# Performance work log

Hardware: AMD Instinct MI355X
Metric: run time of the kernel (lower is better)

## Reference

```python
import jax, jax.numpy as jnp
import numpy as np

HEADS = 8


def setup_inputs() -> dict:
    key = jax.random.key(0)
    ks = jax.random.split(key, 6)
    B, N, D = 4, 2048, 512
    return {
        "x": jax.random.normal(ks[0], (B, N, D), dtype=jnp.float32),
        "pos": jax.random.uniform(ks[1], (B, N, 3), dtype=jnp.float32),
        "qkv_w": jax.random.normal(ks[2], (3 * D, D), dtype=jnp.float32) * 0.02,
        "qkv_b": jax.random.normal(ks[3], (3 * D,), dtype=jnp.float32) * 0.02,
        "out_w": jax.random.normal(ks[4], (D, D), dtype=jnp.float32) * 0.02,
        "out_b": jax.random.normal(ks[5], (D,), dtype=jnp.float32) * 0.02,
    }


def reference(x, pos, qkv_w, qkv_b, out_w, out_b):
    B, N, D = x.shape
    H = HEADS
    Dh = D // H
    scale = D ** (-0.5)  # NOTE: original uses full dim, not head dim

    # QKV projection -> [3, B, H, N, Dh]
    qkv = (x @ qkv_w.T + qkv_b).reshape(B, N, 3, H, Dh).transpose(2, 0, 3, 1, 4)
    q, k, v = qkv[0], qkv[1], qkv[2]

    # partial 3D RoPE on first 6 head dims (3 axis pairs)
    theta = pos * jnp.pi                    # [B, N, 3]
    sin = jnp.sin(theta)[:, None]           # [B, 1, N, 3] broadcasts over heads
    cos = jnp.cos(theta)[:, None]

    def rotate(t):
        x_rot = t[..., :6]
        x1 = x_rot[..., 0::2]               # [B, H, N, 3]
        x2 = x_rot[..., 1::2]
        return jnp.concatenate(
            [x1 * cos - x2 * sin, x1 * sin + x2 * cos, t[..., 6:]], axis=-1
        )

    q = rotate(q)
    k = rotate(k)

    attn = jax.nn.softmax(jnp.einsum("bhqd,bhkd->bhqk", q, k) * scale, axis=-1)
    out = jnp.einsum("bhqk,bhkd->bhqd", attn, v)          # [B, H, N, Dh]
    out = out.transpose(0, 2, 1, 3).reshape(B, N, D)
    return out @ out_w.T + out_b
```

## Files before the change

### kernel.cpp

```cpp
#include <hip/hip_runtime.h>
#include <stdint.h>

typedef __attribute__((ext_vector_type(4))) float f32x4;
typedef __attribute__((ext_vector_type(16))) float f32x16;
typedef __attribute__((ext_vector_type(8))) short bf16x8;
typedef __attribute__((ext_vector_type(4))) unsigned short u16x4;

__device__ __forceinline__ unsigned short f2bf(float f) {
    unsigned int u = __builtin_bit_cast(unsigned int, f);
    u += 0x7fffu + ((u >> 16) & 1u);
    return (unsigned short)(u >> 16);
}
__device__ __forceinline__ float bf2f(unsigned short s) {
    unsigned int u = ((unsigned int)s) << 16;
    return __builtin_bit_cast(float, u);
}
__device__ __forceinline__ float fexp2(float x) {
#if __has_builtin(__builtin_amdgcn_exp2f)
    return __builtin_amdgcn_exp2f(x);
#else
    return exp2f(x);
#endif
}
__device__ __forceinline__ unsigned int cvt_pk_bf16(float lo, float hi) {
    unsigned int r;
    asm("v_cvt_pk_bf16_f32 %0, %1, %2" : "=v"(r) : "v"(lo), "v"(hi));
    return r;
}

__global__ void k_cvt3(const float* __restrict__ x,
                       const float* __restrict__ w1,
                       const float* __restrict__ w2,
                       unsigned short* __restrict__ out) {
    const int C1 = 1048576;
    const int C2 = 196608;
    int i = blockIdx.x * blockDim.x + threadIdx.x;
    f32x4 v;
    if (i < C1)            v = ((const f32x4*)x)[i];
    else if (i < C1 + C2)  v = ((const f32x4*)w1)[i - C1];
    else                   v = ((const f32x4*)w2)[i - C1 - C2];
    u16x4 o;
    o.x = f2bf(v.x); o.y = f2bf(v.y); o.z = f2bf(v.z); o.w = f2bf(v.w);
    ((u16x4*)out)[i] = o;
}

template<int OUT_BF16>
__global__ __launch_bounds__(256, 2)
void k_gemm_nt(const unsigned short* __restrict__ A,
               const unsigned short* __restrict__ Bm,
               const float* __restrict__ bias,
               void* __restrict__ Cout, int M, int N, int K) {
    __shared__ unsigned short As[128 * 64];
    __shared__ unsigned short Bs[128 * 64];
    const int tid = threadIdx.x;
    const int lane = tid & 63;
    const int w = tid >> 6;
    const int wr = (w >> 1) * 64, wc = (w & 1) * 64;
    const int g = lane >> 4, fr = lane & 15;

    f32x4 acc[4][4];
#pragma unroll
    for (int i = 0; i < 4; ++i)
#pragma unroll
        for (int j = 0; j < 4; ++j) acc[i][j] = f32x4{0.f, 0.f, 0.f, 0.f};

    const int srow8 = lane >> 3;
    const int swc = ((lane & 7) ^ srow8) * 8;
    const unsigned short* Abase = A + (size_t)(blockIdx.x * 128 + w * 8 + srow8) * K + swc;
    const unsigned short* Bbase = Bm + (size_t)(blockIdx.y * 128 + w * 8 + srow8) * K + swc;
    char* ldsA = (char*)As + w * 1024;
    char* ldsB = (char*)Bs + w * 1024;

    for (int k0 = 0; k0 < K; k0 += 64) {
        __syncthreads();
#pragma unroll
        for (int i = 0; i < 4; ++i) {
            __builtin_amdgcn_global_load_lds(
                (const __attribute__((address_space(1))) void*)(Abase + (size_t)i * 32 * K + k0),
                (__attribute__((address_space(3))) void*)(ldsA + i * 4096), 16, 0, 0);
            __builtin_amdgcn_global_load_lds(
                (const __attribute__((address_space(1))) void*)(Bbase + (size_t)i * 32 * K + k0),
                (__attribute__((address_space(3))) void*)(ldsB + i * 4096), 16, 0, 0);
        }
        __syncthreads();
        bf16x8 af[2][4], bfv[2][4];
#pragma unroll
        for (int kk = 0; kk < 2; ++kk) {
#pragma unroll
            for (int mi = 0; mi < 4; ++mi)
                af[kk][mi] = *(const bf16x8*)&As[(wr + mi * 16 + fr) * 64 + (((kk * 4 + g) ^ (fr & 7)) * 8)];
#pragma unroll
            for (int ni = 0; ni < 4; ++ni)
                bfv[kk][ni] = *(const bf16x8*)&Bs[(wc + ni * 16 + fr) * 64 + (((kk * 4 + g) ^ (fr & 7)) * 8)];
        }
#pragma unroll
        for (int kk = 0; kk < 2; ++kk)
#pragma unroll
            for (int mi = 0; mi < 4; ++mi)
#pragma unroll
                for (int ni = 0; ni < 4; ++ni)
                    acc[mi][ni] = __builtin_amdgcn_mfma_f32_16x16x32_bf16(af[kk][mi], bfv[kk][ni], acc[mi][ni], 0, 0, 0);
    }

#pragma unroll
    for (int mi = 0; mi < 4; ++mi) {
#pragma unroll
        for (int ni = 0; ni < 4; ++ni) {
            int row = blockIdx.x * 128 + wr + mi * 16 + g * 4;
            int col = blockIdx.y * 128 + wc + ni * 16 + fr;
            float bz = bias[col];
#pragma unroll
            for (int r = 0; r < 4; ++r) {
                float v = acc[mi][ni][r] + bz;
                if (OUT_BF16) ((unsigned short*)Cout)[(size_t)(row + r) * N + col] = f2bf(v);
                else          ((float*)Cout)[(size_t)(row + r) * N + col] = v;
            }
        }
    }
}

__global__ void k_rotary(const unsigned short* __restrict__ qkv,
                         const float* __restrict__ pos,
                         unsigned short* __restrict__ Qb,
                         unsigned short* __restrict__ Kb,
                         unsigned short* __restrict__ VT) {
    const float PI = 3.14159265358979323846f;
    const float QS = 0.04419417382415922f * 1.44269504088896341f;
    int cid = blockIdx.x * 256 + threadIdx.x;
    int s = cid >> 19;
    int r = cid & 524287;
    if (s < 2) {
        int m = r >> 6, c = r & 63;
        int h = c >> 3, dc = c & 7;
        int b = m >> 11, n = m & 2047;
        bf16x8 v = *(const bf16x8*)&qkv[m * 1536 + s * 512 + c * 8];
        float f[8];
#pragma unroll
        for (int i = 0; i < 8; ++i) f[i] = bf2f((unsigned short)v[i]);
        if (dc == 0) {
            float nf[6];
#pragma unroll
            for (int j = 0; j < 3; ++j) {
                float th = pos[m * 3 + j] * PI;
                float sn = __sinf(th), cs = __cosf(th);
                float x1 = f[2 * j], x2 = f[2 * j + 1];
                nf[j] = x1 * cs - x2 * sn;
                nf[3 + j] = x1 * sn + x2 * cs;
            }
#pragma unroll
            for (int j = 0; j < 6; ++j) f[j] = nf[j];
        }
        if (s == 0) {
#pragma unroll
            for (int i = 0; i < 8; ++i) f[i] *= QS;
        }
        bf16x8 o;
#pragma unroll
        for (int i = 0; i < 8; ++i) o[i] = (short)f2bf(f[i]);
        unsigned short* dst = (s == 0) ? Qb : Kb;
        *(bf16x8*)&dst[((size_t)(b * 8 + h) * 2048 + n) * 64 + dc * 8] = o;
    } else {
        int cd = r >> 13;
        int m = r & 8191;
        int b = m >> 11, n = m & 2047;
        int h = cd >> 3, d8 = (cd & 7) * 8;
        bf16x8 v = *(const bf16x8*)&qkv[m * 1536 + 1024 + cd * 8];
        int q2 = (n >> 2) & 3;
        int np = n + (q2 == 1 ? 4 : (q2 == 2 ? -4 : 0));
        size_t base = ((size_t)(b * 8 + h) * 64 + d8) * 2048 + np;
#pragma unroll
        for (int i = 0; i < 8; ++i) VT[base + (size_t)i * 2048] = (unsigned short)v[i];
    }
}

__global__ __launch_bounds__(512, 4)
void k_attn(const unsigned short* __restrict__ Qb,
            const unsigned short* __restrict__ Kb,
            const unsigned short* __restrict__ VT,
            unsigned short* __restrict__ Ob) {
    __shared__ unsigned short smem[2][2][2][4096];
    const int tid = threadIdx.x, lane = tid & 63, w = tid >> 6;
    const int wl = w & 3, half = w >> 2;
    const int l31 = lane & 31, hi = lane >> 5;
    const int bid = blockIdx.x;
    const int bh = (bid & 7) * 4 + ((bid >> 3) >> 4);
    const int qb = (bid >> 3) & 15;
    const int b = bh >> 3, h = bh & 7;
    const int qr0 = qb * 128 + wl * 32;
    const unsigned short* Q = Qb + (size_t)bh * 2048 * 64;
    const unsigned short* K = Kb + (size_t)bh * 2048 * 64;
    const unsigned short* V = VT + (size_t)bh * 64 * 2048;
    const int thalf = half * 16;

    const int srow8 = lane >> 3;
    const int swc = ((lane & 7) ^ srow8) << 3;
    const int sA = wl, sB = wl + 4;

    bf16x8 bq[4];
#pragma unroll
    for (int ds = 0; ds < 4; ++ds)
        bq[ds] = *(const bf16x8*)&Q[(size_t)(qr0 + l31) * 64 + ds * 16 + hi * 8];

    f32x16 oT0, oT1;
#pragma unroll
    for (int i = 0; i < 16; ++i) { oT0[i] = 0.f; oT1[i] = 0.f; }
    float lpart = 0.f;

    auto stage = [&](int bsel, int t) {
        const int kv0 = t * 64;
        const unsigned short* k0 = K + (size_t)(kv0 + sA * 8 + srow8) * 64 + swc;
        const unsigned short* k1 = K + (size_t)(kv0 + sB * 8 + srow8) * 64 + swc;
        const unsigned short* v0 = V + (size_t)(sA * 8 + srow8) * 2048 + kv0 + swc;
        const unsigned short* v1 = V + (size_t)(sB * 8 + srow8) * 2048 + kv0 + swc;
        char* dk = (char*)&smem[half][0][bsel][0];
        char* dv = (char*)&smem[half][1][bsel][0];
        __builtin_amdgcn_global_load_lds((const __attribute__((address_space(1))) void*)k0,
                                         (__attribute__((address_space(3))) void*)(dk + sA * 1024), 16, 0, 0);
        __builtin_amdgcn_global_load_lds((const __attribute__((address_space(1))) void*)k1,
                                         (__attribute__((address_space(3))) void*)(dk + sB * 1024), 16, 0, 0);
        __builtin_amdgcn_global_load_lds((const __attribute__((address_space(1))) void*)v0,
                                         (__attribute__((address_space(3))) void*)(dv + sA * 1024), 16, 0, 0);
        __builtin_amdgcn_global_load_lds((const __attribute__((address_space(1))) void*)v1,
                                         (__attribute__((address_space(3))) void*)(dv + sB * 1024), 16, 0, 0);
    };

    auto pack8 = [&](const float* p) -> bf16x8 {
        union { unsigned int u[4]; bf16x8 v; } c;
        c.u[0] = cvt_pk_bf16(p[0], p[1]);
        c.u[1] = cvt_pk_bf16(p[2], p[3]);
        c.u[2] = cvt_pk_bf16(p[4], p[5]);
        c.u[3] = cvt_pk_bf16(p[6], p[7]);
        return c.v;
    };

    auto compute = [&](int bsel) {
        const unsigned short* KsC = &smem[half][0][bsel][0];
        const unsigned short* VtC = &smem[half][1][bsel][0];
        f32x16 s0, s1;
#pragma unroll
        for (int i = 0; i < 16; ++i) { s0[i] = 0.f; s1[i] = 0.f; }
        __builtin_amdgcn_s_setprio(1);
#pragma unroll
        for (int ds = 0; ds < 4; ++ds) {
            const int c = ((((ds << 1) | hi) ^ (l31 & 7)) << 3);
            bf16x8 ka0 = *(const bf16x8*)&KsC[l31 * 64 + c];
            bf16x8 ka1 = *(const bf16x8*)&KsC[(32 + l31) * 64 + c];
            s0 = __builtin_amdgcn_mfma_f32_32x32x16_bf16(ka0, bq[ds], s0, 0, 0, 0);
            s1 = __builtin_amdgcn_mfma_f32_32x32x16_bf16(ka1, bq[ds], s1, 0, 0, 0);
        }
        __builtin_amdgcn_s_setprio(0);
        float p0[16], p1[16];
        float lsum = 0.f;
#pragma unroll
        for (int r = 0; r < 16; ++r) {
            p0[r] = fexp2(s0[r]);
            p1[r] = fexp2(s1[r]);
            lsum += p0[r] + p1[r];
        }
        lpart += lsum;
        bf16x8 pb0 = pack8(p0);
        bf16x8 pb1 = pack8(p0 + 8);
        bf16x8 pb2 = pack8(p1);
        bf16x8 pb3 = pack8(p1 + 8);
        __builtin_amdgcn_s_setprio(1);
#pragma unroll
        for (int kb = 0; kb < 4; ++kb) {
            const int c = ((((kb << 1) | hi) ^ (l31 & 7)) << 3);
            bf16x8 av0 = *(const bf16x8*)&VtC[l31 * 64 + c];
            bf16x8 av1 = *(const bf16x8*)&VtC[(32 + l31) * 64 + c];
            bf16x8 pbk = (kb == 0) ? pb0 : (kb == 1) ? pb1 : (kb == 2) ? pb2 : pb3;
            oT0 = __builtin_amdgcn_mfma_f32_32x32x16_bf16(av0, pbk, oT0, 0, 0, 0);
            oT1 = __builtin_amdgcn_mfma_f32_32x32x16_bf16(av1, pbk, oT1, 0, 0, 0);
        }
        __builtin_amdgcn_s_setprio(0);
    };

    stage(0, thalf);
    int cur = 0;
#pragma unroll 1
    for (int t = 0; t < 15; ++t) {
        __builtin_amdgcn_s_barrier();
        stage(cur ^ 1, thalf + t + 1);
        asm volatile("s_waitcnt vmcnt(4)" ::: "memory");
        __builtin_amdgcn_s_barrier();
        compute(cur);
        cur ^= 1;
    }
    asm volatile("s_waitcnt vmcnt(0)" ::: "memory");
    __builtin_amdgcn_s_barrier();
    compute(cur);

    __syncthreads();
    float* mrg = (float*)&smem[0][0][0][0];
    float* slot = mrg + (size_t)(wl * 64 + lane) * 33;
    if (half) {
#pragma unroll
        for (int i = 0; i < 16; ++i) { slot[i] = oT0[i]; slot[16 + i] = oT1[i]; }
        slot[32] = lpart;
    }
    __syncthreads();
    if (!half) {
#pragma unroll
        for (int i = 0; i < 16; ++i) { oT0[i] += slot[i]; oT1[i] += slot[16 + i]; }
        float lf = lpart + slot[32];
        lf += __shfl_xor(lf, 32, 64);
        float il = 1.f / lf;
        size_t rowbase = (size_t)(b * 2048 + qr0 + l31) * 512 + h * 64;
#pragma unroll
        for (int grp = 0; grp < 4; ++grp) {
            u16x4 o0, o1;
#pragma unroll
            for (int i = 0; i < 4; ++i) {
                o0[i] = f2bf(oT0[grp * 4 + i] * il);
                o1[i] = f2bf(oT1[grp * 4 + i] * il);
            }
            int dv0 = grp * 8 + 4 * hi;
            *(u16x4*)&Ob[rowbase + dv0] = o0;
            *(u16x4*)&Ob[rowbase + 32 + dv0] = o1;
        }
    }
}

extern "C" void kernel_launch(void* const* d_in, const int* in_sizes, int n_in,
                              void* d_out, int out_size, void* d_ws, size_t ws_size,
                              hipStream_t stream) {
    const float* x     = (const float*)d_in[0];
    const float* pos   = (const float*)d_in[1];
    const float* qkv_w = (const float*)d_in[2];
    const float* qkv_b = (const float*)d_in[3];
    const float* out_w = (const float*)d_in[4];
    const float* out_b = (const float*)d_in[5];
    float* out = (float*)d_out;

    unsigned short* Xb   = (unsigned short*)d_ws;
    unsigned short* W1b  = Xb   + (size_t)8192 * 512;
    unsigned short* W2b  = W1b  + (size_t)1536 * 512;
    unsigned short* QKVb = W2b  + (size_t)512 * 512;
    unsigned short* Qb   = QKVb + (size_t)8192 * 1536;
    unsigned short* Kb   = Qb   + (size_t)4194304;
    unsigned short* VTb  = Kb   + (size_t)4194304;
    unsigned short* Ob   = VTb  + (size_t)4194304;

    k_cvt3<<<5120, 256, 0, stream>>>(x, qkv_w, out_w, Xb);
    k_gemm_nt<1><<<dim3(64, 12), 256, 0, stream>>>(Xb, W1b, qkv_b, QKVb, 8192, 1536, 512);
    k_rotary<<<6144, 256, 0, stream>>>(QKVb, pos, Qb, Kb, VTb);
    k_attn<<<512, 512, 0, stream>>>(Qb, Kb, VTb, Ob);
    k_gemm_nt<0><<<dim3(64, 4), 256, 0, stream>>>(Ob, W2b, out_b, out, 8192, 512, 512);
}
```

Baseline: 91.84 us.

## Double-buffer GEMM LDS tiles and load attention V directly into registers

The GEMM kernel gets two LDS buffers per operand, so the next K tile's global-to-LDS copy is issued before the current tile is computed, plus s_setprio around the MFMAs. The attention kernel stops staging V through LDS. Each wave loads its V fragments from global memory straight into registers one tile ahead, with hand-placed vmcnt waits that overlap them with the QK MFMAs. This aims to hide load latency and cut LDS traffic and footprint. The cost is more LDS per GEMM block, more registers in attention, and vmcnt counts that are fragile.

```diff
diff --git a/kernel.cpp b/kernel.cpp
--- a/kernel.cpp
+++ b/kernel.cpp
@@ -50,8 +50,8 @@
                const unsigned short* __restrict__ Bm,
                const float* __restrict__ bias,
                void* __restrict__ Cout, int M, int N, int K) {
-    __shared__ unsigned short As[128 * 64];
-    __shared__ unsigned short Bs[128 * 64];
+    __shared__ unsigned short As[2][128 * 64];
+    __shared__ unsigned short Bs[2][128 * 64];
     const int tid = threadIdx.x;
     const int lane = tid & 63;
     const int w = tid >> 6;
@@ -68,11 +68,10 @@
     const int swc = ((lane & 7) ^ srow8) * 8;
     const unsigned short* Abase = A + (size_t)(blockIdx.x * 128 + w * 8 + srow8) * K + swc;
     const unsigned short* Bbase = Bm + (size_t)(blockIdx.y * 128 + w * 8 + srow8) * K + swc;
-    char* ldsA = (char*)As + w * 1024;
-    char* ldsB = (char*)Bs + w * 1024;
-
-    for (int k0 = 0; k0 < K; k0 += 64) {
-        __syncthreads();
+
+    auto stage = [&](int bsel, int k0) {
+        char* ldsA = (char*)&As[bsel][0] + w * 1024;
+        char* ldsB = (char*)&Bs[bsel][0] + w * 1024;
 #pragma unroll
         for (int i = 0; i < 4; ++i) {
             __builtin_amdgcn_global_load_lds(
@@ -82,17 +81,19 @@
                 (const __attribute__((address_space(1))) void*)(Bbase + (size_t)i * 32 * K + k0),
                 (__attribute__((address_space(3))) void*)(ldsB + i * 4096), 16, 0, 0);
         }
-        __syncthreads();
+    };
+    auto compute = [&](int bsel) {
         bf16x8 af[2][4], bfv[2][4];
 #pragma unroll
         for (int kk = 0; kk < 2; ++kk) {
 #pragma unroll
             for (int mi = 0; mi < 4; ++mi)
-                af[kk][mi] = *(const bf16x8*)&As[(wr + mi * 16 + fr) * 64 + (((kk * 4 + g) ^ (fr & 7)) * 8)];
+                af[kk][mi] = *(const bf16x8*)&As[bsel][(wr + mi * 16 + fr) * 64 + (((kk * 4 + g) ^ (fr & 7)) * 8)];
 #pragma unroll
             for (int ni = 0; ni < 4; ++ni)
-                bfv[kk][ni] = *(const bf16x8*)&Bs[(wc + ni * 16 + fr) * 64 + (((kk * 4 + g) ^ (fr & 7)) * 8)];
-        }
+                bfv[kk][ni] = *(const bf16x8*)&Bs[bsel][(wc + ni * 16 + fr) * 64 + (((kk * 4 + g) ^ (fr & 7)) * 8)];
+        }
+        __builtin_amdgcn_s_setprio(1);
 #pragma unroll
         for (int kk = 0; kk < 2; ++kk)
 #pragma unroll
@@ -100,7 +101,24 @@
 #pragma unroll
                 for (int ni = 0; ni < 4; ++ni)
                     acc[mi][ni] = __builtin_amdgcn_mfma_f32_16x16x32_bf16(af[kk][mi], bfv[kk][ni], acc[mi][ni], 0, 0, 0);
-    }
+        __builtin_amdgcn_s_setprio(0);
+    };
+
+    const int nt = K >> 6;
+    stage(0, 0);
+    int cur = 0;
+#pragma unroll 1
+    for (int t = 0; t < nt - 1; ++t) {
+        __builtin_amdgcn_s_barrier();
+        stage(cur ^ 1, (t + 1) << 6);
+        asm volatile("s_waitcnt vmcnt(8)" ::: "memory");
+        __builtin_amdgcn_s_barrier();
+        compute(cur);
+        cur ^= 1;
+    }
+    asm volatile("s_waitcnt vmcnt(0)" ::: "memory");
+    __builtin_amdgcn_s_barrier();
+    compute(cur);
 
 #pragma unroll
     for (int mi = 0; mi < 4; ++mi) {
@@ -178,7 +196,8 @@
             const unsigned short* __restrict__ Kb,
             const unsigned short* __restrict__ VT,
             unsigned short* __restrict__ Ob) {
-    __shared__ unsigned short smem[2][2][2][4096];
+    __shared__ __align__(16) char smemraw[33792];
+    unsigned short (*Ksm)[2][4096] = (unsigned short (*)[2][4096])smemraw;
     const int tid = threadIdx.x, lane = tid & 63, w = tid >> 6;
     const int wl = w & 3, half = w >> 2;
     const int l31 = lane & 31, hi = lane >> 5;
@@ -206,22 +225,25 @@
     for (int i = 0; i < 16; ++i) { oT0[i] = 0.f; oT1[i] = 0.f; }
     float lpart = 0.f;
 
-    auto stage = [&](int bsel, int t) {
+    auto stageK = [&](int bsel, int t) {
         const int kv0 = t * 64;
         const unsigned short* k0 = K + (size_t)(kv0 + sA * 8 + srow8) * 64 + swc;
         const unsigned short* k1 = K + (size_t)(kv0 + sB * 8 + srow8) * 64 + swc;
-        const unsigned short* v0 = V + (size_t)(sA * 8 + srow8) * 2048 + kv0 + swc;
-        const unsigned short* v1 = V + (size_t)(sB * 8 + srow8) * 2048 + kv0 + swc;
-        char* dk = (char*)&smem[half][0][bsel][0];
-        char* dv = (char*)&smem[half][1][bsel][0];
+        char* dk = (char*)&Ksm[half][bsel][0];
         __builtin_amdgcn_global_load_lds((const __attribute__((address_space(1))) void*)k0,
                                          (__attribute__((address_space(3))) void*)(dk + sA * 1024), 16, 0, 0);
         __builtin_amdgcn_global_load_lds((const __attribute__((address_space(1))) void*)k1,
                                          (__attribute__((address_space(3))) void*)(dk + sB * 1024), 16, 0, 0);
-        __builtin_amdgcn_global_load_lds((const __attribute__((address_space(1))) void*)v0,
-                                         (__attribute__((address_space(3))) void*)(dv + sA * 1024), 16, 0, 0);
-        __builtin_amdgcn_global_load_lds((const __attribute__((address_space(1))) void*)v1,
-                                         (__attribute__((address_space(3))) void*)(dv + sB * 1024), 16, 0, 0);
+    };
+
+    bf16x8 va0[4], va1[4];
+    auto loadV = [&](int t) {
+        const int kv0 = t * 64;
+#pragma unroll
+        for (int kb = 0; kb < 4; ++kb) {
+            va0[kb] = *(const bf16x8*)&V[(size_t)l31 * 2048 + kv0 + kb * 16 + hi * 8];
+            va1[kb] = *(const bf16x8*)&V[(size_t)(32 + l31) * 2048 + kv0 + kb * 16 + hi * 8];
+        }
     };
 
     auto pack8 = [&](const float* p) -> bf16x8 {
@@ -233,9 +255,22 @@
         return c.v;
     };
 
-    auto compute = [&](int bsel) {
-        const unsigned short* KsC = &smem[half][0][bsel][0];
-        const unsigned short* VtC = &smem[half][1][bsel][0];
+    stageK(0, thalf);
+    asm volatile("" ::: "memory");
+    loadV(thalf);
+    asm volatile("" ::: "memory");
+    int cur = 0;
+#pragma unroll 1
+    for (int t = 0; t < 16; ++t) {
+        __builtin_amdgcn_s_barrier();
+        if (t < 15) {
+            stageK(cur ^ 1, thalf + t + 1);
+            asm volatile("s_waitcnt vmcnt(10)" ::: "memory");
+        } else {
+            asm volatile("s_waitcnt vmcnt(8)" ::: "memory");
+        }
+        __builtin_amdgcn_s_barrier();
+        const unsigned short* KsC = &Ksm[half][cur][0];
         f32x16 s0, s1;
 #pragma unroll
         for (int i = 0; i < 16; ++i) { s0[i] = 0.f; s1[i] = 0.f; }
@@ -249,6 +284,8 @@
             s1 = __builtin_amdgcn_mfma_f32_32x32x16_bf16(ka1, bq[ds], s1, 0, 0, 0);
         }
         __builtin_amdgcn_s_setprio(0);
+        if (t < 15) asm volatile("s_waitcnt vmcnt(2)" ::: "memory");
+        else        asm volatile("s_waitcnt vmcnt(0)" ::: "memory");
         float p0[16], p1[16];
         float lsum = 0.f;
 #pragma unroll
@@ -265,33 +302,20 @@
         __builtin_amdgcn_s_setprio(1);
 #pragma unroll
         for (int kb = 0; kb < 4; ++kb) {
-            const int c = ((((kb << 1) | hi) ^ (l31 & 7)) << 3);
-            bf16x8 av0 = *(const bf16x8*)&VtC[l31 * 64 + c];
-            bf16x8 av1 = *(const bf16x8*)&VtC[(32 + l31) * 64 + c];
             bf16x8 pbk = (kb == 0) ? pb0 : (kb == 1) ? pb1 : (kb == 2) ? pb2 : pb3;
-            oT0 = __builtin_amdgcn_mfma_f32_32x32x16_bf16(av0, pbk, oT0, 0, 0, 0);
-            oT1 = __builtin_amdgcn_mfma_f32_32x32x16_bf16(av1, pbk, oT1, 0, 0, 0);
+            oT0 = __builtin_amdgcn_mfma_f32_32x32x16_bf16(va0[kb], pbk, oT0, 0, 0, 0);
+            oT1 = __builtin_amdgcn_mfma_f32_32x32x16_bf16(va1[kb], pbk, oT1, 0, 0, 0);
         }
         __builtin_amdgcn_s_setprio(0);
-    };
-
-    stage(0, thalf);
-    int cur = 0;
-#pragma unroll 1
-    for (int t = 0; t < 15; ++t) {
-        __builtin_amdgcn_s_barrier();
-        stage(cur ^ 1, thalf + t + 1);
-        asm volatile("s_waitcnt vmcnt(4)" ::: "memory");
-        __builtin_amdgcn_s_barrier();
-        compute(cur);
+        if (t < 15) {
+            loadV(thalf + t + 1);
+            asm volatile("" ::: "memory");
+        }
         cur ^= 1;
     }
-    asm volatile("s_waitcnt vmcnt(0)" ::: "memory");
-    __builtin_amdgcn_s_barrier();
-    compute(cur);
 
     __syncthreads();
-    float* mrg = (float*)&smem[0][0][0][0];
+    float* mrg = (float*)smemraw;
     float* slot = mrg + (size_t)(wl * 64 + lane) * 33;
     if (half) {
 #pragma unroll
```

After: 168.5 us. 83.4% more time.

## Double-buffer GEMM LDS tiles to overlap global loads with MFMA compute

Applied to the files above, without the earlier changes.

Converts the NT GEMM main loop to a two-stage LDS ping-pong: the next K tile is issued via global_load_lds into the alternate buffer before computing the current one, with explicit vmcnt waits and raw s_barrier calls. It also raises wave priority around the MFMA block with s_setprio. This aims to hide global memory latency behind matrix math. In exchange, LDS per block doubles to 64 KB, which may limit occupancy at two blocks per CU, and it relies on hand-placed waitcnt and barrier ordering for correctness.

```diff
diff --git a/kernel.cpp b/kernel.cpp
--- a/kernel.cpp
+++ b/kernel.cpp
@@ -50,8 +50,8 @@
                const unsigned short* __restrict__ Bm,
                const float* __restrict__ bias,
                void* __restrict__ Cout, int M, int N, int K) {
-    __shared__ unsigned short As[128 * 64];
-    __shared__ unsigned short Bs[128 * 64];
+    __shared__ unsigned short As[2][128 * 64];
+    __shared__ unsigned short Bs[2][128 * 64];
     const int tid = threadIdx.x;
     const int lane = tid & 63;
     const int w = tid >> 6;
@@ -68,11 +68,10 @@
     const int swc = ((lane & 7) ^ srow8) * 8;
     const unsigned short* Abase = A + (size_t)(blockIdx.x * 128 + w * 8 + srow8) * K + swc;
     const unsigned short* Bbase = Bm + (size_t)(blockIdx.y * 128 + w * 8 + srow8) * K + swc;
-    char* ldsA = (char*)As + w * 1024;
-    char* ldsB = (char*)Bs + w * 1024;
-
-    for (int k0 = 0; k0 < K; k0 += 64) {
-        __syncthreads();
+
+    auto stage = [&](int bsel, int k0) {
+        char* ldsA = (char*)&As[bsel][0] + w * 1024;
+        char* ldsB = (char*)&Bs[bsel][0] + w * 1024;
 #pragma unroll
         for (int i = 0; i < 4; ++i) {
             __builtin_amdgcn_global_load_lds(
@@ -82,17 +81,19 @@
                 (const __attribute__((address_space(1))) void*)(Bbase + (size_t)i * 32 * K + k0),
                 (__attribute__((address_space(3))) void*)(ldsB + i * 4096), 16, 0, 0);
         }
-        __syncthreads();
+    };
+    auto compute = [&](int bsel) {
         bf16x8 af[2][4], bfv[2][4];
 #pragma unroll
         for (int kk = 0; kk < 2; ++kk) {
 #pragma unroll
             for (int mi = 0; mi < 4; ++mi)
-                af[kk][mi] = *(const bf16x8*)&As[(wr + mi * 16 + fr) * 64 + (((kk * 4 + g) ^ (fr & 7)) * 8)];
+                af[kk][mi] = *(const bf16x8*)&As[bsel][(wr + mi * 16 + fr) * 64 + (((kk * 4 + g) ^ (fr & 7)) * 8)];
 #pragma unroll
             for (int ni = 0; ni < 4; ++ni)
-                bfv[kk][ni] = *(const bf16x8*)&Bs[(wc + ni * 16 + fr) * 64 + (((kk * 4 + g) ^ (fr & 7)) * 8)];
-        }
+                bfv[kk][ni] = *(const bf16x8*)&Bs[bsel][(wc + ni * 16 + fr) * 64 + (((kk * 4 + g) ^ (fr & 7)) * 8)];
+        }
+        __builtin_amdgcn_s_setprio(1);
 #pragma unroll
         for (int kk = 0; kk < 2; ++kk)
 #pragma unroll
@@ -100,7 +101,24 @@
 #pragma unroll
                 for (int ni = 0; ni < 4; ++ni)
                     acc[mi][ni] = __builtin_amdgcn_mfma_f32_16x16x32_bf16(af[kk][mi], bfv[kk][ni], acc[mi][ni], 0, 0, 0);
-    }
+        __builtin_amdgcn_s_setprio(0);
+    };
+
+    const int nt = K >> 6;
+    stage(0, 0);
+    int cur = 0;
+#pragma unroll 1
+    for (int t = 0; t < nt - 1; ++t) {
+        __builtin_amdgcn_s_barrier();
+        stage(cur ^ 1, (t + 1) << 6);
+        asm volatile("s_waitcnt vmcnt(8)" ::: "memory");
+        __builtin_amdgcn_s_barrier();
+        compute(cur);
+        cur ^= 1;
+    }
+    asm volatile("s_waitcnt vmcnt(0)" ::: "memory");
+    __builtin_amdgcn_s_barrier();
+    compute(cur);
 
 #pragma unroll
     for (int mi = 0; mi < 4; ++mi) {
```

After: 96.03 us. 4.6% more time.
